# Performance work log

Hardware: AMD Instinct MI355X
Metric: run time of the kernel (lower is better)

The kernel has to match this reference:

```python
import jax, jax.numpy as jnp
import numpy as np

NODE = 112
B = 4096
L1, L2, L3, L4 = 256, 256, 128, 64


def setup_inputs() -> dict:
    key = jax.random.key(0)
    ks = jax.random.split(key, 13)
    def lin(kw, kb, fan_in, fan_out):
        bound = 1.0 / np.sqrt(fan_in)
        W = jax.random.uniform(kw, (fan_out, fan_in), jnp.float32, -bound, bound)
        b = jax.random.uniform(kb, (fan_out,), jnp.float32, -bound, bound)
        return W, b
    x = jax.random.normal(ks[0], (B, NODE, NODE), jnp.float32)
    W1, b1 = lin(ks[1], ks[2], NODE, L1)
    W2, b2 = lin(ks[3], ks[4], L1, L2)
    W3, b3 = lin(ks[5], ks[6], L2, L3)
    W4, b4 = lin(ks[7], ks[8], L3, L4)
    W5, b5 = lin(ks[9], ks[10], L4, 1)
    Wf, bf = lin(ks[11], ks[12], NODE, 1)
    return {"x": x, "W1": W1, "b1": b1, "W2": W2, "b2": b2,
            "W3": W3, "b3": b3, "W4": W4, "b4": b4,
            "W5": W5, "b5": b5, "Wf": Wf, "bf": bf}


def reference(x, W1, b1, W2, b2, W3, b3, W4, b4, W5, b5, Wf, bf):
    # bmm(x, eye) == x, so first aggregation is the identity on x.
    h = x  # [B, node, node]
    # layer: aggregate via x, project, relu
    def layer(h, W, b):
        h = jnp.einsum('bnm,bmd->bnd', x, h)  # adjacency aggregation
        return jax.nn.relu(h @ W.T + b)
    h = jax.nn.relu(h @ W1.T + b1)            # first bmm is identity
    h = layer(h, W2, b2)
    h = layer(h, W3, b3)
    h = layer(h, W4, b4)
    h = layer(h, W5, b5)                      # [B, node, 1]
    h = h.reshape(h.shape[0], -1)             # [B, node]
    return h @ Wf.T + bf                      # [B, 1]
```

## Files before the change

kernel.cpp:

```cpp
#include <hip/hip_runtime.h>
#include <hip/hip_bf16.h>


#define NODE 112
#define NBATCH 4096
#define SXS 120
#define AB_OFF (96*SXS)
#define SMEM_BYTES ((AB_OFF + 112*256)*2)

typedef float  f4v   __attribute__((ext_vector_type(4)));
typedef float  f16v  __attribute__((ext_vector_type(16)));
typedef __bf16 bf8v  __attribute__((ext_vector_type(8)));
typedef short  s8v   __attribute__((ext_vector_type(8)));
typedef unsigned u4v __attribute__((ext_vector_type(4)));
typedef unsigned short ushort_t;

__device__ __forceinline__ ushort_t f2bf(float f) {
  union { float f; unsigned u; } v; v.f = f;
  unsigned r = v.u + 0x7FFFu + ((v.u >> 16) & 1u);
  return (ushort_t)(r >> 16);
}
__device__ __forceinline__ float bf2f(ushort_t h) {
  union { unsigned u; float f; } v; v.u = ((unsigned)h) << 16; return v.f;
}
__device__ __forceinline__ unsigned pk2(float a, float b) {
  unsigned short ul = __builtin_bit_cast(unsigned short, (__bf16)a);
  unsigned short uh = __builtin_bit_cast(unsigned short, (__bf16)b);
  return (unsigned)ul | ((unsigned)uh << 16);
}
__device__ __forceinline__ bf8v ld_frag(const ushort_t* p) {
  s8v t = *(const s8v*)p;
  return __builtin_bit_cast(bf8v, t);
}
__device__ __forceinline__ unsigned xchg32(unsigned v, int lane) {
  return (unsigned)__builtin_amdgcn_ds_bpermute(((lane ^ 32) << 2), (int)v);
}
#define MFMA32(a,b,c) __builtin_amdgcn_mfma_f32_32x32x16_bf16((a),(b),(c),0,0,0)

__device__ __forceinline__ void exch_build(const f16v* acc, float bv, int lane,
                                           unsigned* fr)
{
  const bool hiH = (lane >> 5) != 0;
  #pragma unroll
  for (int m=0;m<4;m++) {
    unsigned P[4][2];
    const int NQ = (m==3) ? 2 : 4;
    #pragma unroll
    for (int q=0;q<4;q++) {
      if (q >= NQ) break;
      float v0 = fmaxf(acc[m][4*q+0]+bv, 0.f);
      float v1 = fmaxf(acc[m][4*q+1]+bv, 0.f);
      float v2 = fmaxf(acc[m][4*q+2]+bv, 0.f);
      float v3 = fmaxf(acc[m][4*q+3]+bv, 0.f);
      P[q][0] = pk2(v0, v1);
      P[q][1] = pk2(v2, v3);
    }
    {
      unsigned s0 = hiH ? P[0][0] : P[1][0];
      unsigned s1 = hiH ? P[0][1] : P[1][1];
      unsigned r0 = xchg32(s0, lane);
      unsigned r1 = xchg32(s1, lane);
      unsigned o0 = hiH ? P[1][0] : P[0][0];
      unsigned o1 = hiH ? P[1][1] : P[0][1];
      fr[8*m+0] = hiH ? r0 : o0;
      fr[8*m+1] = hiH ? r1 : o1;
      fr[8*m+2] = hiH ? o0 : r0;
      fr[8*m+3] = hiH ? o1 : r1;
    }
    if (m < 3) {
      unsigned s0 = hiH ? P[2][0] : P[3][0];
      unsigned s1 = hiH ? P[2][1] : P[3][1];
      unsigned r0 = xchg32(s0, lane);
      unsigned r1 = xchg32(s1, lane);
      unsigned o0 = hiH ? P[3][0] : P[2][0];
      unsigned o1 = hiH ? P[3][1] : P[2][1];
      fr[8*m+4] = hiH ? r0 : o0;
      fr[8*m+5] = hiH ? r1 : o1;
      fr[8*m+6] = hiH ? o0 : r0;
      fr[8*m+7] = hiH ? o1 : r1;
    }
  }
}

__device__ __forceinline__ void proj1_exch(
    const ushort_t* Xs, const bf8v* Xr3, const ushort_t* __restrict__ Wg,
    const float* __restrict__ bias, int nt, int lane, unsigned* fr)
{
  const int l31 = lane & 31, h32 = lane >> 5;
  f16v acc[4];
  #pragma unroll
  for (int m=0;m<4;m++)
    #pragma unroll
    for (int r=0;r<16;r++) acc[m][r] = 0.f;

  const ushort_t* aP = Xs + l31*SXS + h32*8;
  const ushort_t* bP = Wg + (nt*32 + l31)*112 + h32*8;
  #pragma unroll
  for (int ks=0; ks<7; ks++) {
    bf8v B = ld_frag(bP + ks*16);
    acc[0] = MFMA32(ld_frag(aP +          ks*16), B, acc[0]);
    acc[1] = MFMA32(ld_frag(aP + 32*SXS + ks*16), B, acc[1]);
    acc[2] = MFMA32(ld_frag(aP + 64*SXS + ks*16), B, acc[2]);
    acc[3] = MFMA32(Xr3[ks], B, acc[3]);
  }
  exch_build(acc, bias[nt*32 + l31], lane, fr);
}

template<int KS>
__device__ __forceinline__ void proj_exch(
    const ushort_t* aBs, const ushort_t* __restrict__ Wg, int WK,
    const float* __restrict__ bias, int nt, int lane, int sw, unsigned* fr)
{
  const int l31 = lane & 31, h32 = lane >> 5;
  f16v acc[4];
  #pragma unroll
  for (int m=0;m<4;m++)
    #pragma unroll
    for (int r=0;r<16;r++) acc[m][r] = 0.f;

  const int r0 = l31*256, r1 = (32+l31)*256, r2 = (64+l31)*256;
  const int r3 = (96 + (l31 & 15))*256;
  const ushort_t* bP = Wg + (nt*32 + l31)*WK + h32*8;
  #pragma unroll
  for (int ks=0; ks<KS; ks++) {
    bf8v B = ld_frag(bP + ks*16);
    const int c = (16*ks + 8*h32) ^ sw;
    acc[0] = MFMA32(ld_frag(aBs + r0 + c), B, acc[0]);
    acc[1] = MFMA32(ld_frag(aBs + r1 + c), B, acc[1]);
    acc[2] = MFMA32(ld_frag(aBs + r2 + c), B, acc[2]);
    acc[3] = MFMA32(ld_frag(aBs + r3 + c), B, acc[3]);
  }
  exch_build(acc, bias[nt*32 + l31], lane, fr);
}

template<int N0>
__device__ __forceinline__ void agg_half(
    const unsigned* fr, const ushort_t* Xs, const bf8v* Xr3,
    ushort_t* aBs, int mt, int lane, int sw)
{
  const int l31 = lane & 31, h32 = lane >> 5;
  f16v acc0, acc1;
  #pragma unroll
  for (int r=0;r<16;r++) { acc0[r] = 0.f; acc1[r] = 0.f; }

  const ushort_t* bP = Xs + l31*SXS + h32*8;
  #pragma unroll
  for (int ks=0; ks<7; ks++) {
    u4v t = (u4v){fr[4*ks+0], fr[4*ks+1], fr[4*ks+2], fr[4*ks+3]};
    bf8v A = __builtin_bit_cast(bf8v, t);
    bf8v B0 = ld_frag(bP + N0*32*SXS + ks*16);
    bf8v B1 = (N0 == 0) ? ld_frag(bP + 32*SXS + ks*16) : Xr3[ks];
    acc0 = MFMA32(A, B0, acc0);
    acc1 = MFMA32(A, B1, acc1);
  }

  #pragma unroll
  for (int s=0;s<2;s++) {
    const f16v& a = s ? acc1 : acc0;
    const int n = N0 + s;
    const int row = (n < 3) ? (n*32 + l31) : (96 + l31);
    const bool on = (n < 3) || (l31 < 16);
    #pragma unroll
    for (int q=0;q<4;q++) {
      uint2 pv;
      pv.x = pk2(a[4*q+0], a[4*q+1]);
      pv.y = pk2(a[4*q+2], a[4*q+3]);
      const int col = (mt*32 + 8*q + 4*h32) ^ sw;
      if (on) *(uint2*)(aBs + row*256 + col) = pv;
    }
  }
}

__global__ void prep_weights(const float* __restrict__ W1, const float* __restrict__ W2,
                             const float* __restrict__ W3, const float* __restrict__ W4,
                             ushort_t* __restrict__ o)
{
  int i = blockIdx.x*256 + threadIdx.x;
  if (i < 28672)       o[i] = f2bf(W1[i]);
  else if (i < 94208)  o[i] = f2bf(W2[i - 28672]);
  else if (i < 126976) o[i] = f2bf(W3[i - 94208]);
  else if (i < 135168) o[i] = f2bf(W4[i - 126976]);
}

__global__ void __launch_bounds__(512, 4) gcn_kernel(
    const float* __restrict__ x, const ushort_t* __restrict__ wsp,
    const float* __restrict__ b1, const float* __restrict__ b2,
    const float* __restrict__ b3, const float* __restrict__ b4,
    const float* __restrict__ W5, const float* __restrict__ b5,
    const float* __restrict__ Wf, const float* __restrict__ bfc,
    float* __restrict__ out)
{
  extern __shared__ ushort_t smem[];
  ushort_t* Xs = smem;
  ushort_t* aB = smem + AB_OFF;

  const int tid  = threadIdx.x;
  const int w    = tid >> 6;
  const int lane = tid & 63;
  const int l31  = lane & 31, h32 = lane >> 5;
  const int sw   = (l31 & 7) << 3;

  {
    const float4* x4 = (const float4*)(x + (size_t)blockIdx.x * (NODE*NODE));
    for (int i = tid; i < (NODE*NODE/4); i += 512) {
      float4 v = x4[i];
      int r = i / 28, c4 = (i - r*28) * 4;
      uint2 pv; pv.x = pk2(v.x, v.y); pv.y = pk2(v.z, v.w);
      ushort_t* dst = (r < 96) ? (Xs + r*SXS + c4) : (aB + (r-96)*SXS + c4);
      *(uint2*)dst = pv;
    }
  }
  __syncthreads();

  bf8v Xr3[7];
  {
    const ushort_t* sp = aB + (l31 & 15)*SXS + h32*8;
    #pragma unroll
    for (int ks=0;ks<7;ks++) Xr3[ks] = ld_frag(sp + ks*16);
  }
  __syncthreads();

  unsigned fr[28];

  proj1_exch(Xs, Xr3, wsp, b1, w, lane, fr);
  agg_half<0>(fr, Xs, Xr3, aB, w, lane, sw);
  agg_half<2>(fr, Xs, Xr3, aB, w, lane, sw);
  __syncthreads();

  proj_exch<16>(aB, wsp + 28672, 256, b2, w, lane, sw, fr);
  __syncthreads();
  agg_half<0>(fr, Xs, Xr3, aB, w, lane, sw);
  agg_half<2>(fr, Xs, Xr3, aB, w, lane, sw);
  __syncthreads();

  if (w < 4) proj_exch<16>(aB, wsp + 94208, 256, b3, w, lane, sw, fr);
  __syncthreads();
  if (w < 4) {
    agg_half<0>(fr, Xs, Xr3, aB, w, lane, sw);
    agg_half<2>(fr, Xs, Xr3, aB, w, lane, sw);
  }
  __syncthreads();

  if (w < 2) proj_exch<8>(aB, wsp + 126976, 128, b4, w, lane, sw, fr);
  __syncthreads();
  if (w < 2) {
    agg_half<0>(fr, Xs, Xr3, aB, w, lane, sw);
    agg_half<2>(fr, Xs, Xr3, aB, w, lane, sw);
  }
  __syncthreads();

  float partial = 0.f;
  if (tid < NODE) {
    const int swr = (tid & 7) << 3;
    const ushort_t* row = aB + tid*256;
    float s = 0.f;
    #pragma unroll
    for (int k4 = 0; k4 < 16; k4++) {
      uint2 u = *(const uint2*)(row + ((4*k4) ^ swr));
      s += bf2f((ushort_t)(u.x & 0xFFFF)) * W5[k4*4+0];
      s += bf2f((ushort_t)(u.x >> 16))    * W5[k4*4+1];
      s += bf2f((ushort_t)(u.y & 0xFFFF)) * W5[k4*4+2];
      s += bf2f((ushort_t)(u.y >> 16))    * W5[k4*4+3];
    }
    s += b5[0];
    s = s > 0.f ? s : 0.f;
    partial = s * Wf[tid];
  }
  float* red = (float*)Xs;
  if (tid < 128) red[tid] = partial;
  __syncthreads();
  if (w == 0) {
    float v = red[lane] + red[lane + 64];
    #pragma unroll
    for (int off = 32; off > 0; off >>= 1)
      v += __shfl_xor(v, off, 64);
    if (lane == 0) out[blockIdx.x] = v + bfc[0];
  }
}

extern "C" void kernel_launch(void* const* d_in, const int* in_sizes, int n_in,
                              void* d_out, int out_size, void* d_ws, size_t ws_size,
                              hipStream_t stream) {
  const float* x   = (const float*)d_in[0];
  const float* W1  = (const float*)d_in[1];
  const float* b1  = (const float*)d_in[2];
  const float* W2  = (const float*)d_in[3];
  const float* b2  = (const float*)d_in[4];
  const float* W3  = (const float*)d_in[5];
  const float* b3  = (const float*)d_in[6];
  const float* W4  = (const float*)d_in[7];
  const float* b4  = (const float*)d_in[8];
  const float* W5  = (const float*)d_in[9];
  const float* b5  = (const float*)d_in[10];
  const float* Wf  = (const float*)d_in[11];
  const float* bfc = (const float*)d_in[12];
  ushort_t* wsp = (ushort_t*)d_ws;
  float* out = (float*)d_out;

  prep_weights<<<528, 256, 0, stream>>>(W1, W2, W3, W4, wsp);

  (void)hipFuncSetAttribute((const void*)gcn_kernel,
                            hipFuncAttributeMaxDynamicSharedMemorySize, SMEM_BYTES);
  gcn_kernel<<<NBATCH, 512, SMEM_BYTES, stream>>>(x, wsp, b1, b2, b3, b4,
                                                  W5, b5, Wf, bfc, out);
}
```

Baseline: 618.1 us.

## Halve block size to 256 threads, each wave handling two column tiles

New measurement: 534.3 us. 13.6% less time.

```diff
diff --git a/kernel.cpp b/kernel.cpp
--- a/kernel.cpp
+++ b/kernel.cpp
@@ -182,7 +182,7 @@
   else if (i < 135168) o[i] = f2bf(W4[i - 126976]);
 }
 
-__global__ void __launch_bounds__(512, 4) gcn_kernel(
+__global__ void __launch_bounds__(256, 2) gcn_kernel(
     const float* __restrict__ x, const ushort_t* __restrict__ wsp,
     const float* __restrict__ b1, const float* __restrict__ b2,
     const float* __restrict__ b3, const float* __restrict__ b4,
@@ -202,7 +202,7 @@
 
   {
     const float4* x4 = (const float4*)(x + (size_t)blockIdx.x * (NODE*NODE));
-    for (int i = tid; i < (NODE*NODE/4); i += 512) {
+    for (int i = tid; i < (NODE*NODE/4); i += 256) {
       float4 v = x4[i];
       int r = i / 28, c4 = (i - r*28) * 4;
       uint2 pv; pv.x = pk2(v.x, v.y); pv.y = pk2(v.z, v.w);
@@ -220,32 +220,36 @@
   }
   __syncthreads();
 
-  unsigned fr[28];
-
-  proj1_exch(Xs, Xr3, wsp, b1, w, lane, fr);
-  agg_half<0>(fr, Xs, Xr3, aB, w, lane, sw);
-  agg_half<2>(fr, Xs, Xr3, aB, w, lane, sw);
-  __syncthreads();
-
-  proj_exch<16>(aB, wsp + 28672, 256, b2, w, lane, sw, fr);
-  __syncthreads();
-  agg_half<0>(fr, Xs, Xr3, aB, w, lane, sw);
-  agg_half<2>(fr, Xs, Xr3, aB, w, lane, sw);
-  __syncthreads();
-
-  if (w < 4) proj_exch<16>(aB, wsp + 94208, 256, b3, w, lane, sw, fr);
-  __syncthreads();
-  if (w < 4) {
-    agg_half<0>(fr, Xs, Xr3, aB, w, lane, sw);
-    agg_half<2>(fr, Xs, Xr3, aB, w, lane, sw);
-  }
-  __syncthreads();
-
-  if (w < 2) proj_exch<8>(aB, wsp + 126976, 128, b4, w, lane, sw, fr);
+  unsigned frA[28], frB[28];
+
+  proj1_exch(Xs, Xr3, wsp, b1, w, lane, frA);
+  agg_half<0>(frA, Xs, Xr3, aB, w, lane, sw);
+  agg_half<2>(frA, Xs, Xr3, aB, w, lane, sw);
+  proj1_exch(Xs, Xr3, wsp, b1, w+4, lane, frB);
+  agg_half<0>(frB, Xs, Xr3, aB, w+4, lane, sw);
+  agg_half<2>(frB, Xs, Xr3, aB, w+4, lane, sw);
+  __syncthreads();
+
+  proj_exch<16>(aB, wsp + 28672, 256, b2, w,   lane, sw, frA);
+  proj_exch<16>(aB, wsp + 28672, 256, b2, w+4, lane, sw, frB);
+  __syncthreads();
+  agg_half<0>(frA, Xs, Xr3, aB, w,   lane, sw);
+  agg_half<2>(frA, Xs, Xr3, aB, w,   lane, sw);
+  agg_half<0>(frB, Xs, Xr3, aB, w+4, lane, sw);
+  agg_half<2>(frB, Xs, Xr3, aB, w+4, lane, sw);
+  __syncthreads();
+
+  proj_exch<16>(aB, wsp + 94208, 256, b3, w, lane, sw, frA);
+  __syncthreads();
+  agg_half<0>(frA, Xs, Xr3, aB, w, lane, sw);
+  agg_half<2>(frA, Xs, Xr3, aB, w, lane, sw);
+  __syncthreads();
+
+  if (w < 2) proj_exch<8>(aB, wsp + 126976, 128, b4, w, lane, sw, frA);
   __syncthreads();
   if (w < 2) {
-    agg_half<0>(fr, Xs, Xr3, aB, w, lane, sw);
-    agg_half<2>(fr, Xs, Xr3, aB, w, lane, sw);
+    agg_half<0>(frA, Xs, Xr3, aB, w, lane, sw);
+    agg_half<2>(frA, Xs, Xr3, aB, w, lane, sw);
   }
   __syncthreads();
 
@@ -301,6 +305,6 @@
 
   (void)hipFuncSetAttribute((const void*)gcn_kernel,
                             hipFuncAttributeMaxDynamicSharedMemorySize, SMEM_BYTES);
-  gcn_kernel<<<NBATCH, 512, SMEM_BYTES, stream>>>(x, wsp, b1, b2, b3, b4,
+  gcn_kernel<<<NBATCH, 256, SMEM_BYTES, stream>>>(x, wsp, b1, b2, b3, b4,
                                                   W5, b5, Wf, bfc, out);
 }
```
